# Performance work log

Measured on AMD Instinct MI355X. Metric: run time of the kernel, lower is better.

Reference implementation:

```python
import jax, jax.numpy as jnp
import numpy as np


def setup_inputs() -> dict:
    key = jax.random.key(0)
    ks = jax.random.split(key, 7)
    B, D = 8192, 4096  # D = 64*64 perfect square
    def lin(k, fan_out, fan_in):
        bound = 1.0 / np.sqrt(fan_in)
        kw, kb = jax.random.split(k)
        W = jax.random.uniform(kw, (fan_out, fan_in), jnp.float32, -bound, bound)
        b = jax.random.uniform(kb, (fan_out,), jnp.float32, -bound, bound)
        return W, b
    W1, b1 = lin(ks[1], 512, D)
    W2, b2 = lin(ks[2], 256, 512)
    W3, b3 = lin(ks[3], D, 256)
    x = jax.random.normal(ks[0], (B, D), jnp.float32)
    return {"x": x, "W1": W1, "b1": b1, "W2": W2, "b2": b2, "W3": W3, "b3": b3}


def column_sort(m):
    # torch: sort dim=1; permute(0,2,1) sort dim=1 permute back == sort axis=2; sort dim=1
    m = jnp.sort(m, axis=1)
    m = jnp.sort(m, axis=2)
    m = jnp.sort(m, axis=1)
    return m


def reference(x, W1, b1, W2, b2, W3, b3):
    B, D = x.shape
    n = int(np.sqrt(D))
    xs = column_sort(x.reshape(B, n, n)).reshape(B, D)
    h = jax.nn.relu(xs @ W1.T + b1)
    h = jax.nn.relu(h @ W2.T + b2)
    return h @ W3.T + b3
```

## Files before the change

### kernel.cpp

```cpp
#include <hip/hip_runtime.h>
#include <hip/hip_bf16.h>


#define B_DIM 8192
#define D_DIM 4096
#define H1_DIM 512
#define H2_DIM 256

typedef __attribute__((ext_vector_type(8))) short bf16x8;
typedef __attribute__((ext_vector_type(4))) float f32x4;

__device__ __forceinline__ unsigned short f2bf(float f) {
    union { float f; unsigned u; } v{f};
    unsigned r = v.u + 0x7FFF + ((v.u >> 16) & 1);
    return (unsigned short)(r >> 16);
}

__device__ __forceinline__ void sort64(float v[64]) {
#pragma unroll
    for (int k = 2; k <= 64; k <<= 1) {
#pragma unroll
        for (int j = k >> 1; j > 0; j >>= 1) {
#pragma unroll
            for (int p = 0; p < 32; ++p) {
                const int i  = ((p & ~(j - 1)) << 1) | (p & (j - 1));
                const int ix = i | j;
                const bool up = ((i & k) == 0);
                float a = v[i], b = v[ix];
                float lo = fminf(a, b), hi = fmaxf(a, b);
                v[i]  = up ? lo : hi;
                v[ix] = up ? hi : lo;
            }
        }
    }
}

__global__ __launch_bounds__(64)
void sort_kernel(const float* __restrict__ x, unsigned short* __restrict__ xs)
{
    __shared__ float lds[64 * 68];
    const int b    = blockIdx.x;
    const int lane = threadIdx.x;
    const float* src = x + (size_t)b * D_DIM;
    unsigned short* dst = xs + (size_t)b * D_DIM;

    float4 t[16];
#pragma unroll
    for (int q = 0; q < 16; ++q)
        t[q] = *(const float4*)(src + (q * 64 + lane) * 4);
#pragma unroll
    for (int q = 0; q < 16; ++q) {
        int f = q * 64 + lane;
        *(float4*)&lds[(f >> 4) * 68 + (f & 15) * 4] = t[q];
    }
    __syncthreads();

    float v[64];
#pragma unroll
    for (int i = 0; i < 64; ++i) v[i] = lds[i * 68 + lane];
    sort64(v);

    __syncthreads();
#pragma unroll
    for (int i = 0; i < 64; ++i) lds[i * 68 + lane] = v[i];
    __syncthreads();
#pragma unroll
    for (int q = 0; q < 16; ++q) {
        float4 r = *(const float4*)&lds[lane * 68 + q * 4];
        v[q * 4 + 0] = r.x; v[q * 4 + 1] = r.y;
        v[q * 4 + 2] = r.z; v[q * 4 + 3] = r.w;
    }
    sort64(v);

    __syncthreads();
#pragma unroll
    for (int q = 0; q < 16; ++q) {
        float4 r;
        r.x = v[q * 4 + 0]; r.y = v[q * 4 + 1];
        r.z = v[q * 4 + 2]; r.w = v[q * 4 + 3];
        *(float4*)&lds[lane * 68 + q * 4] = r;
    }
    __syncthreads();
#pragma unroll
    for (int i = 0; i < 64; ++i) v[i] = lds[i * 68 + lane];
    sort64(v);

    __syncthreads();
#pragma unroll
    for (int i = 0; i < 64; ++i) lds[i * 68 + lane] = v[i];
    __syncthreads();
#pragma unroll
    for (int q = 0; q < 16; ++q) {
        int f = q * 64 + lane;
        float4 r = *(const float4*)&lds[(f >> 4) * 68 + (f & 15) * 4];
        ushort4 o;
        o.x = f2bf(r.x); o.y = f2bf(r.y); o.z = f2bf(r.z); o.w = f2bf(r.w);
        *(ushort4*)(dst + f * 4) = o;
    }
}

__global__ __launch_bounds__(256)
void cvt_bf16(const float* __restrict__ src, unsigned short* __restrict__ dst, int n4)
{
    int i = blockIdx.x * blockDim.x + threadIdx.x;
    if (i < n4) {
        float4 v = ((const float4*)src)[i];
        ushort4 o;
        o.x = f2bf(v.x); o.y = f2bf(v.y); o.z = f2bf(v.z); o.w = f2bf(v.w);
        ((ushort4*)dst)[i] = o;
    }
}

template<int BM, int BN, bool RELU, bool OUT_BF16>
__global__ __launch_bounds__(256, 2)
void gemm_mfma(const unsigned short* __restrict__ A,
               const unsigned short* __restrict__ Wt,
               const float* __restrict__ bias,
               void* __restrict__ Cout, int M, int N, int K)
{
    constexpr int BK  = 64;
    constexpr int WTM = BM / 2, WTN = BN / 2;
    constexpr int FM  = WTM / 16, FN = WTN / 16;
    __shared__ unsigned short sA[BM * BK];
    __shared__ unsigned short sB[BN * BK];

    const int tid  = threadIdx.x;
    const int wave = tid >> 6;
    const int lane = tid & 63;
    const int wm   = wave >> 1, wn = wave & 1;
    const int gm0  = blockIdx.y * BM;
    const int gn0  = blockIdx.x * BN;

    const int r_in = lane >> 3;
    const int j_in = lane & 7;

    f32x4 acc[FM][FN] = {};

    for (int k0 = 0; k0 < K; k0 += BK) {
#pragma unroll
        for (int c = 0; c < BM / 32; ++c) {
            int rb  = wave * (BM / 4) + c * 8;
            int r   = rb + r_in;
            int seg = j_in ^ (r & 7);
            const unsigned short* g = A + (size_t)(gm0 + r) * K + k0 + seg * 8;
            __builtin_amdgcn_global_load_lds(
                (const __attribute__((address_space(1))) void*)g,
                (__attribute__((address_space(3))) void*)&sA[rb * 64],
                16, 0, 0);
        }
#pragma unroll
        for (int c = 0; c < BN / 32; ++c) {
            int rb  = wave * (BN / 4) + c * 8;
            int r   = rb + r_in;
            int seg = j_in ^ (r & 7);
            const unsigned short* g = Wt + (size_t)(gn0 + r) * K + k0 + seg * 8;
            __builtin_amdgcn_global_load_lds(
                (const __attribute__((address_space(1))) void*)g,
                (__attribute__((address_space(3))) void*)&sB[rb * 64],
                16, 0, 0);
        }
        __syncthreads();

#pragma unroll
        for (int ks = 0; ks < 2; ++ks) {
            bf16x8 afr[FM], bfr[FN];
#pragma unroll
            for (int i = 0; i < FM; ++i) {
                int m   = wm * WTM + i * 16 + (lane & 15);
                int seg = (ks * 4 + (lane >> 4)) ^ (m & 7);
                afr[i] = *(const bf16x8*)&sA[m * 64 + seg * 8];
            }
#pragma unroll
            for (int j = 0; j < FN; ++j) {
                int n   = wn * WTN + j * 16 + (lane & 15);
                int seg = (ks * 4 + (lane >> 4)) ^ (n & 7);
                bfr[j] = *(const bf16x8*)&sB[n * 64 + seg * 8];
            }
#pragma unroll
            for (int i = 0; i < FM; ++i)
#pragma unroll
                for (int j = 0; j < FN; ++j)
                    acc[i][j] = __builtin_amdgcn_mfma_f32_16x16x32_bf16(
                        afr[i], bfr[j], acc[i][j], 0, 0, 0);
        }
        __syncthreads();
    }

#pragma unroll
    for (int j = 0; j < FN; ++j) {
        int n = gn0 + wn * WTN + j * 16 + (lane & 15);
        float bv = bias[n];
#pragma unroll
        for (int i = 0; i < FM; ++i) {
#pragma unroll
            for (int r = 0; r < 4; ++r) {
                int m = gm0 + wm * WTM + i * 16 + (lane >> 4) * 4 + r;
                float v = acc[i][j][r] + bv;
                if (RELU) v = fmaxf(v, 0.f);
                if (OUT_BF16)
                    ((unsigned short*)Cout)[(size_t)m * N + n] = f2bf(v);
                else
                    ((float*)Cout)[(size_t)m * N + n] = v;
            }
        }
    }
}

extern "C" void kernel_launch(void* const* d_in, const int* in_sizes, int n_in,
                              void* d_out, int out_size, void* d_ws, size_t ws_size,
                              hipStream_t stream)
{
    const float* x  = (const float*)d_in[0];
    const float* W1 = (const float*)d_in[1];
    const float* b1 = (const float*)d_in[2];
    const float* W2 = (const float*)d_in[3];
    const float* b2 = (const float*)d_in[4];
    const float* W3 = (const float*)d_in[5];
    const float* b3 = (const float*)d_in[6];
    float* out = (float*)d_out;

    unsigned short* xs = (unsigned short*)d_out;
    char* ws = (char*)d_ws;
    unsigned short* h1b = (unsigned short*)(ws);
    unsigned short* h2b = (unsigned short*)(ws + (8u  << 20));
    unsigned short* W1b = (unsigned short*)(ws + (12u << 20));
    unsigned short* W2b = (unsigned short*)(ws + (16u << 20));
    unsigned short* W3b = (unsigned short*)(ws + (17u << 20));

    cvt_bf16<<<(H1_DIM * D_DIM / 4 + 255) / 256, 256, 0, stream>>>(W1, W1b, H1_DIM * D_DIM / 4);
    cvt_bf16<<<(H2_DIM * H1_DIM / 4 + 255) / 256, 256, 0, stream>>>(W2, W2b, H2_DIM * H1_DIM / 4);
    cvt_bf16<<<(D_DIM * H2_DIM / 4 + 255) / 256, 256, 0, stream>>>(W3, W3b, D_DIM * H2_DIM / 4);

    sort_kernel<<<B_DIM, 64, 0, stream>>>(x, xs);

    gemm_mfma<128, 64, true, true>
        <<<dim3(H1_DIM / 64, B_DIM / 128), 256, 0, stream>>>(
            xs, W1b, b1, h1b, B_DIM, H1_DIM, D_DIM);

    gemm_mfma<64, 64, true, true>
        <<<dim3(H2_DIM / 64, B_DIM / 64), 256, 0, stream>>>(
            h1b, W2b, b2, h2b, B_DIM, H2_DIM, H1_DIM);

    gemm_mfma<128, 128, false, false>
        <<<dim3(D_DIM / 128, B_DIM / 128), 256, 0, stream>>>(
            h2b, W3b, b3, out, B_DIM, D_DIM, H2_DIM);
}
```

Measured before the change: 391.7 us.

## Sort bf16 order-preserving keys with packed 16-bit min/max network

```diff
diff --git a/kernel.cpp b/kernel.cpp
--- a/kernel.cpp
+++ b/kernel.cpp
@@ -7,6 +7,9 @@
 #define H1_DIM 512
 #define H2_DIM 256
 
+typedef unsigned short u16;
+typedef __attribute__((ext_vector_type(2))) unsigned short u16x2;
+typedef __attribute__((ext_vector_type(2))) short i16x2;
 typedef __attribute__((ext_vector_type(8))) short bf16x8;
 typedef __attribute__((ext_vector_type(4))) float f32x4;
 
@@ -15,86 +18,138 @@
     unsigned r = v.u + 0x7FFF + ((v.u >> 16) & 1);
     return (unsigned short)(r >> 16);
 }
-
-__device__ __forceinline__ void sort64(float v[64]) {
+__device__ __forceinline__ u16 fkey(float f) {
+    u16 bf = f2bf(f);
+    u16 m  = (u16)(((short)bf) >> 15);
+    return (u16)(bf ^ (m | 0x8000));
+}
+__device__ __forceinline__ u16x2 mk2(u16 a, u16 b) { u16x2 r; r.x = a; r.y = b; return r; }
+
+#if defined(__has_builtin) && __has_builtin(__builtin_elementwise_min)
+__device__ __forceinline__ u16x2 pkmin(u16x2 a, u16x2 b) { return __builtin_elementwise_min(a, b); }
+__device__ __forceinline__ u16x2 pkmax(u16x2 a, u16x2 b) { return __builtin_elementwise_max(a, b); }
+#else
+__device__ __forceinline__ u16x2 pkmin(u16x2 a, u16x2 b) {
+    return mk2(a.x < b.x ? a.x : b.x, a.y < b.y ? a.y : b.y);
+}
+__device__ __forceinline__ u16x2 pkmax(u16x2 a, u16x2 b) {
+    return mk2(a.x > b.x ? a.x : b.x, a.y > b.y ? a.y : b.y);
+}
+#endif
+
+__device__ __forceinline__ void sortnet(u16x2 v[32]) {
 #pragma unroll
     for (int k = 2; k <= 64; k <<= 1) {
 #pragma unroll
-        for (int j = k >> 1; j > 0; j >>= 1) {
-#pragma unroll
-            for (int p = 0; p < 32; ++p) {
-                const int i  = ((p & ~(j - 1)) << 1) | (p & (j - 1));
-                const int ix = i | j;
-                const bool up = ((i & k) == 0);
-                float a = v[i], b = v[ix];
-                float lo = fminf(a, b), hi = fmaxf(a, b);
-                v[i]  = up ? lo : hi;
-                v[ix] = up ? hi : lo;
+        for (int j = k >> 1; j >= 1; j >>= 1) {
+            if (j == 32) {
+#pragma unroll
+                for (int p = 0; p < 32; ++p) {
+                    u16x2 sw = mk2(v[p].y, v[p].x);
+                    u16x2 mn = pkmin(v[p], sw), mx = pkmax(v[p], sw);
+                    v[p] = mk2(mn.x, mx.y);
+                }
+            } else {
+#pragma unroll
+                for (int p = 0; p < 32; ++p) {
+                    if (p & j) continue;
+                    const int q = p | j;
+                    const bool upx = ((p & k) == 0);
+                    const bool upy = (((p + 32) & k) == 0);
+                    u16x2 mn = pkmin(v[p], v[q]), mx = pkmax(v[p], v[q]);
+                    if (upx == upy) {
+                        v[p] = upx ? mn : mx;
+                        v[q] = upx ? mx : mn;
+                    } else {
+                        v[p] = mk2(mn.x, mx.y);
+                        v[q] = mk2(mx.x, mn.y);
+                    }
+                }
             }
         }
     }
 }
 
-__global__ __launch_bounds__(64)
-void sort_kernel(const float* __restrict__ x, unsigned short* __restrict__ xs)
+#define SRT 66
+__global__ __launch_bounds__(128)
+void sort_kernel(const float* __restrict__ x, u16* __restrict__ xs)
 {
-    __shared__ float lds[64 * 68];
-    const int b    = blockIdx.x;
-    const int lane = threadIdx.x;
-    const float* src = x + (size_t)b * D_DIM;
-    unsigned short* dst = xs + (size_t)b * D_DIM;
+    __shared__ u16 smem[2 * 64 * SRT];
+    const int wave = threadIdx.x >> 6;
+    const int lane = threadIdx.x & 63;
+    u16* s = smem + wave * 64 * SRT;
+    const int b = blockIdx.x * 2 + wave;
+    const float* src = x  + (size_t)b * D_DIM;
+    u16*         dst = xs + (size_t)b * D_DIM;
 
     float4 t[16];
 #pragma unroll
-    for (int q = 0; q < 16; ++q)
-        t[q] = *(const float4*)(src + (q * 64 + lane) * 4);
-#pragma unroll
-    for (int q = 0; q < 16; ++q) {
-        int f = q * 64 + lane;
-        *(float4*)&lds[(f >> 4) * 68 + (f & 15) * 4] = t[q];
-    }
-    __syncthreads();
-
-    float v[64];
-#pragma unroll
-    for (int i = 0; i < 64; ++i) v[i] = lds[i * 68 + lane];
-    sort64(v);
-
-    __syncthreads();
-#pragma unroll
-    for (int i = 0; i < 64; ++i) lds[i * 68 + lane] = v[i];
-    __syncthreads();
-#pragma unroll
-    for (int q = 0; q < 16; ++q) {
-        float4 r = *(const float4*)&lds[lane * 68 + q * 4];
-        v[q * 4 + 0] = r.x; v[q * 4 + 1] = r.y;
-        v[q * 4 + 2] = r.z; v[q * 4 + 3] = r.w;
-    }
-    sort64(v);
-
-    __syncthreads();
-#pragma unroll
-    for (int q = 0; q < 16; ++q) {
-        float4 r;
-        r.x = v[q * 4 + 0]; r.y = v[q * 4 + 1];
-        r.z = v[q * 4 + 2]; r.w = v[q * 4 + 3];
-        *(float4*)&lds[lane * 68 + q * 4] = r;
-    }
-    __syncthreads();
-#pragma unroll
-    for (int i = 0; i < 64; ++i) v[i] = lds[i * 68 + lane];
-    sort64(v);
-
-    __syncthreads();
-#pragma unroll
-    for (int i = 0; i < 64; ++i) lds[i * 68 + lane] = v[i];
-    __syncthreads();
-#pragma unroll
-    for (int q = 0; q < 16; ++q) {
-        int f = q * 64 + lane;
-        float4 r = *(const float4*)&lds[(f >> 4) * 68 + (f & 15) * 4];
-        ushort4 o;
-        o.x = f2bf(r.x); o.y = f2bf(r.y); o.z = f2bf(r.z); o.w = f2bf(r.w);
+    for (int qq = 0; qq < 16; ++qq)
+        t[qq] = *(const float4*)(src + (qq * 64 + lane) * 4);
+#pragma unroll
+    for (int qq = 0; qq < 16; ++qq) {
+        int f = qq * 64 + lane, r = f >> 4, c0 = (f & 15) * 4;
+        *(u16x2*)&s[r * SRT + c0]     = mk2(fkey(t[qq].x), fkey(t[qq].y));
+        *(u16x2*)&s[r * SRT + c0 + 2] = mk2(fkey(t[qq].z), fkey(t[qq].w));
+    }
+    __syncthreads();
+
+    u16x2 v[32];
+#pragma unroll
+    for (int p = 0; p < 32; ++p)
+        v[p] = mk2(s[p * SRT + lane], s[(p + 32) * SRT + lane]);
+    sortnet(v);
+
+    __syncthreads();
+    {
+        const int pos = (lane & 31) * 2 + (lane >> 5);
+#pragma unroll
+        for (int p = 0; p < 32; ++p) {
+            s[p * SRT + pos]        = v[p].x;
+            s[(p + 32) * SRT + pos] = v[p].y;
+        }
+    }
+    __syncthreads();
+
+#pragma unroll
+    for (int p = 0; p < 32; ++p)
+        v[p] = *(const u16x2*)&s[lane * SRT + p * 2];
+    sortnet(v);
+
+    __syncthreads();
+#pragma unroll
+    for (int p = 0; p < 32; ++p) {
+        s[lane * SRT + p]      = v[p].x;
+        s[lane * SRT + p + 32] = v[p].y;
+    }
+    __syncthreads();
+
+#pragma unroll
+    for (int p = 0; p < 32; ++p)
+        v[p] = mk2(s[p * SRT + lane], s[(p + 32) * SRT + lane]);
+    sortnet(v);
+
+#pragma unroll
+    for (int p = 0; p < 32; ++p) {
+        i16x2 sh = ((i16x2)v[p]) >> 15;
+        u16x2 m  = (u16x2)sh;
+        u16x2 c8; c8.x = 0x8000; c8.y = 0x8000;
+        v[p] = v[p] ^ ((~m) | c8);
+    }
+
+    __syncthreads();
+#pragma unroll
+    for (int p = 0; p < 32; ++p) {
+        s[p * SRT + lane]        = v[p].x;
+        s[(p + 32) * SRT + lane] = v[p].y;
+    }
+    __syncthreads();
+#pragma unroll
+    for (int qq = 0; qq < 16; ++qq) {
+        int f = qq * 64 + lane, r = f >> 4, c0 = (f & 15) * 4;
+        u16x2 a = *(const u16x2*)&s[r * SRT + c0];
+        u16x2 c = *(const u16x2*)&s[r * SRT + c0 + 2];
+        ushort4 o; o.x = a.x; o.y = a.y; o.z = c.x; o.w = c.y;
         *(ushort4*)(dst + f * 4) = o;
     }
 }
@@ -219,7 +274,7 @@
     const float* b3 = (const float*)d_in[6];
     float* out = (float*)d_out;
 
-    unsigned short* xs = (unsigned short*)d_out;
+    u16* xs = (u16*)d_out;
     char* ws = (char*)d_ws;
     unsigned short* h1b = (unsigned short*)(ws);
     unsigned short* h2b = (unsigned short*)(ws + (8u  << 20));
@@ -227,18 +282,18 @@
     unsigned short* W2b = (unsigned short*)(ws + (16u << 20));
     unsigned short* W3b = (unsigned short*)(ws + (17u << 20));
 
+    sort_kernel<<<B_DIM / 2, 128, 0, stream>>>(x, xs);
+
     cvt_bf16<<<(H1_DIM * D_DIM / 4 + 255) / 256, 256, 0, stream>>>(W1, W1b, H1_DIM * D_DIM / 4);
     cvt_bf16<<<(H2_DIM * H1_DIM / 4 + 255) / 256, 256, 0, stream>>>(W2, W2b, H2_DIM * H1_DIM / 4);
     cvt_bf16<<<(D_DIM * H2_DIM / 4 + 255) / 256, 256, 0, stream>>>(W3, W3b, D_DIM * H2_DIM / 4);
 
-    sort_kernel<<<B_DIM, 64, 0, stream>>>(x, xs);
-
     gemm_mfma<128, 64, true, true>
         <<<dim3(H1_DIM / 64, B_DIM / 128), 256, 0, stream>>>(
             xs, W1b, b1, h1b, B_DIM, H1_DIM, D_DIM);
 
-    gemm_mfma<64, 64, true, true>
-        <<<dim3(H2_DIM / 64, B_DIM / 64), 256, 0, stream>>>(
+    gemm_mfma<128, 64, true, true>
+        <<<dim3(H2_DIM / 64, B_DIM / 128), 256, 0, stream>>>(
             h1b, W2b, b2, h2b, B_DIM, H2_DIM, H1_DIM);
 
     gemm_mfma<128, 128, false, false>
```

New measurement: 388.8 us. No clear change (-0.7%).

## Sort two rows per block using packed bf16 keys with pk_min/max

Applied to the files above, without the earlier changes.

```diff
diff --git a/kernel.cpp b/kernel.cpp
--- a/kernel.cpp
+++ b/kernel.cpp
@@ -7,100 +7,139 @@
 #define H1_DIM 512
 #define H2_DIM 256
 
+typedef unsigned int u32;
+typedef unsigned short u16;
+typedef __attribute__((ext_vector_type(2))) short i16x2;
 typedef __attribute__((ext_vector_type(8))) short bf16x8;
 typedef __attribute__((ext_vector_type(4))) float f32x4;
 
-__device__ __forceinline__ unsigned short f2bf(float f) {
+__device__ __forceinline__ u16 f2bf(float f) {
     union { float f; unsigned u; } v{f};
     unsigned r = v.u + 0x7FFF + ((v.u >> 16) & 1);
-    return (unsigned short)(r >> 16);
-}
-
-__device__ __forceinline__ void sort64(float v[64]) {
+    return (u16)(r >> 16);
+}
+
+__device__ __forceinline__ u32 pkmin(u32 a, u32 b) {
+    u32 d; asm("v_pk_min_u16 %0, %1, %2" : "=v"(d) : "v"(a), "v"(b)); return d;
+}
+__device__ __forceinline__ u32 pkmax(u32 a, u32 b) {
+    u32 d; asm("v_pk_max_u16 %0, %1, %2" : "=v"(d) : "v"(a), "v"(b)); return d;
+}
+__device__ __forceinline__ u32 pkashr15(u32 a) {
+    union { u32 u; i16x2 v; } x; x.u = a;
+    x.v = x.v >> 15;
+    return x.u;
+}
+
+__device__ __forceinline__ u32 key2(float fa, float fb) {
+    union { __hip_bfloat162 h; u32 u; } cv;
+    cv.h = __float22bfloat162_rn(float2{fa, fb});
+    u32 bb = cv.u;
+    return bb ^ (pkashr15(bb) | 0x80008000u);
+}
+
+__device__ __forceinline__ void sortnet64(u32 v[64]) {
 #pragma unroll
     for (int k = 2; k <= 64; k <<= 1) {
 #pragma unroll
         for (int j = k >> 1; j > 0; j >>= 1) {
 #pragma unroll
-            for (int p = 0; p < 32; ++p) {
-                const int i  = ((p & ~(j - 1)) << 1) | (p & (j - 1));
-                const int ix = i | j;
+            for (int i = 0; i < 64; ++i) {
+                if (i & j) continue;
+                const int q = i | j;
                 const bool up = ((i & k) == 0);
-                float a = v[i], b = v[ix];
-                float lo = fminf(a, b), hi = fmaxf(a, b);
-                v[i]  = up ? lo : hi;
-                v[ix] = up ? hi : lo;
+                u32 mn = pkmin(v[i], v[q]);
+                u32 mx = pkmax(v[i], v[q]);
+                v[i] = up ? mn : mx;
+                v[q] = up ? mx : mn;
             }
         }
     }
 }
 
 __global__ __launch_bounds__(64)
-void sort_kernel(const float* __restrict__ x, unsigned short* __restrict__ xs)
-{
-    __shared__ float lds[64 * 68];
+void sort_kernel(const float* __restrict__ x, u16* __restrict__ xs)
+{
+    __shared__ u32 S[64 * 64];
+    const int lane = threadIdx.x;
     const int b    = blockIdx.x;
-    const int lane = threadIdx.x;
-    const float* src = x + (size_t)b * D_DIM;
-    unsigned short* dst = xs + (size_t)b * D_DIM;
-
-    float4 t[16];
-#pragma unroll
-    for (int q = 0; q < 16; ++q)
-        t[q] = *(const float4*)(src + (q * 64 + lane) * 4);
+    const float4* A4 = (const float4*)(x + (size_t)(2 * b)     * D_DIM);
+    const float4* B4 = (const float4*)(x + (size_t)(2 * b + 1) * D_DIM);
+    u16* dstA = xs + (size_t)(2 * b)     * D_DIM;
+    u16* dstB = xs + (size_t)(2 * b + 1) * D_DIM;
+
 #pragma unroll
     for (int q = 0; q < 16; ++q) {
         int f = q * 64 + lane;
-        *(float4*)&lds[(f >> 4) * 68 + (f & 15) * 4] = t[q];
-    }
-    __syncthreads();
-
-    float v[64];
-#pragma unroll
-    for (int i = 0; i < 64; ++i) v[i] = lds[i * 68 + lane];
-    sort64(v);
-
-    __syncthreads();
-#pragma unroll
-    for (int i = 0; i < 64; ++i) lds[i * 68 + lane] = v[i];
-    __syncthreads();
-#pragma unroll
-    for (int q = 0; q < 16; ++q) {
-        float4 r = *(const float4*)&lds[lane * 68 + q * 4];
-        v[q * 4 + 0] = r.x; v[q * 4 + 1] = r.y;
-        v[q * 4 + 2] = r.z; v[q * 4 + 3] = r.w;
-    }
-    sort64(v);
-
-    __syncthreads();
-#pragma unroll
-    for (int q = 0; q < 16; ++q) {
-        float4 r;
-        r.x = v[q * 4 + 0]; r.y = v[q * 4 + 1];
-        r.z = v[q * 4 + 2]; r.w = v[q * 4 + 3];
-        *(float4*)&lds[lane * 68 + q * 4] = r;
-    }
-    __syncthreads();
-#pragma unroll
-    for (int i = 0; i < 64; ++i) v[i] = lds[i * 68 + lane];
-    sort64(v);
-
-    __syncthreads();
-#pragma unroll
-    for (int i = 0; i < 64; ++i) lds[i * 68 + lane] = v[i];
-    __syncthreads();
+        float4 a = A4[f], c = B4[f];
+        int r = f >> 4, s = f & 15;
+        uint4 w;
+        w.x = key2(a.x, c.x); w.y = key2(a.y, c.y);
+        w.z = key2(a.z, c.z); w.w = key2(a.w, c.w);
+        *(uint4*)(S + r * 64 + ((s ^ (r & 15)) << 2)) = w;
+    }
+    __syncthreads();
+
+    u32 v[64];
+#pragma unroll
+    for (int p = 0; p < 64; ++p)
+        v[p] = S[p * 64 + (((lane >> 2) ^ (p & 15)) << 2) + (lane & 3)];
+    sortnet64(v);
+    __syncthreads();
+#pragma unroll
+    for (int p = 0; p < 64; ++p)
+        S[p * 64 + (((lane >> 2) ^ (p & 15)) << 2) + (lane & 3)] = v[p];
+    __syncthreads();
+
+#pragma unroll
+    for (int q = 0; q < 16; ++q) {
+        uint4 w = *(const uint4*)(S + lane * 64 + ((q ^ (lane & 15)) << 2));
+        v[4 * q + 0] = w.x; v[4 * q + 1] = w.y;
+        v[4 * q + 2] = w.z; v[4 * q + 3] = w.w;
+    }
+    sortnet64(v);
+    __syncthreads();
+#pragma unroll
+    for (int q = 0; q < 16; ++q) {
+        uint4 w;
+        w.x = v[4 * q + 0]; w.y = v[4 * q + 1];
+        w.z = v[4 * q + 2]; w.w = v[4 * q + 3];
+        *(uint4*)(S + lane * 64 + ((q ^ (lane & 15)) << 2)) = w;
+    }
+    __syncthreads();
+
+#pragma unroll
+    for (int p = 0; p < 64; ++p)
+        v[p] = S[p * 64 + (((lane >> 2) ^ (p & 15)) << 2) + (lane & 3)];
+    sortnet64(v);
+
+#pragma unroll
+    for (int p = 0; p < 64; ++p)
+        v[p] = v[p] ^ (~pkashr15(v[p]) | 0x80008000u);
+
+    __syncthreads();
+#pragma unroll
+    for (int p = 0; p < 64; ++p)
+        S[p * 64 + (((lane >> 2) ^ (p & 15)) << 2) + (lane & 3)] = v[p];
+    __syncthreads();
+
 #pragma unroll
     for (int q = 0; q < 16; ++q) {
         int f = q * 64 + lane;
-        float4 r = *(const float4*)&lds[(f >> 4) * 68 + (f & 15) * 4];
-        ushort4 o;
-        o.x = f2bf(r.x); o.y = f2bf(r.y); o.z = f2bf(r.z); o.w = f2bf(r.w);
-        *(ushort4*)(dst + f * 4) = o;
+        int r = f >> 4, s = f & 15;
+        uint4 w = *(const uint4*)(S + r * 64 + ((s ^ (r & 15)) << 2));
+        uint2 oa, ob;
+        oa.x = (w.x & 0xFFFFu) | (w.y << 16);
+        oa.y = (w.z & 0xFFFFu) | (w.w << 16);
+        ob.x = (w.x >> 16) | (w.y & 0xFFFF0000u);
+        ob.y = (w.z >> 16) | (w.w & 0xFFFF0000u);
+        *(uint2*)(dstA + r * 64 + s * 4) = oa;
+        *(uint2*)(dstB + r * 64 + s * 4) = ob;
     }
 }
 
 __global__ __launch_bounds__(256)
-void cvt_bf16(const float* __restrict__ src, unsigned short* __restrict__ dst, int n4)
+void cvt_bf16(const float* __restrict__ src, u16* __restrict__ dst, int n4)
 {
     int i = blockIdx.x * blockDim.x + threadIdx.x;
     if (i < n4) {
@@ -112,17 +151,16 @@
 }
 
 template<int BM, int BN, bool RELU, bool OUT_BF16>
-__global__ __launch_bounds__(256, 2)
-void gemm_mfma(const unsigned short* __restrict__ A,
-               const unsigned short* __restrict__ Wt,
-               const float* __restrict__ bias,
-               void* __restrict__ Cout, int M, int N, int K)
+__device__ __forceinline__
+void gemm_body(const u16* __restrict__ A, const u16* __restrict__ Wt,
+               const float* __restrict__ bias, void* __restrict__ Cout,
+               int M, int N, int K)
 {
     constexpr int BK  = 64;
     constexpr int WTM = BM / 2, WTN = BN / 2;
     constexpr int FM  = WTM / 16, FN = WTN / 16;
-    __shared__ unsigned short sA[BM * BK];
-    __shared__ unsigned short sB[BN * BK];
+    __shared__ u16 sA[BM * BK];
+    __shared__ u16 sB[BN * BK];
 
     const int tid  = threadIdx.x;
     const int wave = tid >> 6;
@@ -142,7 +180,7 @@
             int rb  = wave * (BM / 4) + c * 8;
             int r   = rb + r_in;
             int seg = j_in ^ (r & 7);
-            const unsigned short* g = A + (size_t)(gm0 + r) * K + k0 + seg * 8;
+            const u16* g = A + (size_t)(gm0 + r) * K + k0 + seg * 8;
             __builtin_amdgcn_global_load_lds(
                 (const __attribute__((address_space(1))) void*)g,
                 (__attribute__((address_space(3))) void*)&sA[rb * 64],
@@ -153,7 +191,7 @@
             int rb  = wave * (BN / 4) + c * 8;
             int r   = rb + r_in;
             int seg = j_in ^ (r & 7);
-            const unsigned short* g = Wt + (size_t)(gn0 + r) * K + k0 + seg * 8;
+            const u16* g = Wt + (size_t)(gn0 + r) * K + k0 + seg * 8;
             __builtin_amdgcn_global_load_lds(
                 (const __attribute__((address_space(1))) void*)g,
                 (__attribute__((address_space(3))) void*)&sB[rb * 64],
@@ -195,16 +233,26 @@
 #pragma unroll
             for (int r = 0; r < 4; ++r) {
                 int m = gm0 + wm * WTM + i * 16 + (lane >> 4) * 4 + r;
-                float v = acc[i][j][r] + bv;
-                if (RELU) v = fmaxf(v, 0.f);
+                float vv = acc[i][j][r] + bv;
+                if (RELU) vv = fmaxf(vv, 0.f);
                 if (OUT_BF16)
-                    ((unsigned short*)Cout)[(size_t)m * N + n] = f2bf(v);
+                    ((u16*)Cout)[(size_t)m * N + n] = f2bf(vv);
                 else
-                    ((float*)Cout)[(size_t)m * N + n] = v;
-            }
-        }
-    }
-}
+                    ((float*)Cout)[(size_t)m * N + n] = vv;
+            }
+        }
+    }
+}
+
+__global__ __launch_bounds__(256, 2)
+void gemm1_xs_w1(const u16* A, const u16* Wt, const float* bias, void* C,
+                 int M, int N, int K) { gemm_body<128, 64, true, true >(A, Wt, bias, C, M, N, K); }
+__global__ __launch_bounds__(256, 2)
+void gemm2_h1_w2(const u16* A, const u16* Wt, const float* bias, void* C,
+                 int M, int N, int K) { gemm_body<128, 64, true, true >(A, Wt, bias, C, M, N, K); }
+__global__ __launch_bounds__(256, 2)
+void gemm3_h2_w3(const u16* A, const u16* Wt, const float* bias, void* C,
+                 int M, int N, int K) { gemm_body<128, 128, false, false>(A, Wt, bias, C, M, N, K); }
 
 extern "C" void kernel_launch(void* const* d_in, const int* in_sizes, int n_in,
                               void* d_out, int out_size, void* d_ws, size_t ws_size,
@@ -217,31 +265,27 @@
     const float* b2 = (const float*)d_in[4];
     const float* W3 = (const float*)d_in[5];
     const float* b3 = (const float*)d_in[6];
-    float* out = (float*)d_out;
-
-    unsigned short* xs = (unsigned short*)d_out;
+
+    u16* xs = (u16*)d_out;
     char* ws = (char*)d_ws;
-    unsigned short* h1b = (unsigned short*)(ws);
-    unsigned short* h2b = (unsigned short*)(ws + (8u  << 20));
-    unsigned short* W1b = (unsigned short*)(ws + (12u << 20));
-    unsigned short* W2b = (unsigned short*)(ws + (16u << 20));
-    unsigned short* W3b = (unsigned short*)(ws + (17u << 20));
+    u16* h1b = (u16*)(ws);
+    u16* h2b = (u16*)(ws + (8u  << 20));
+    u16* W1b = (u16*)(ws + (12u << 20));
+    u16* W2b = (u16*)(ws + (16u << 20));
+    u16* W3b = (u16*)(ws + (17u << 20));
+
+    sort_kernel<<<B_DIM / 2, 64, 0, stream>>>(x, xs);
 
     cvt_bf16<<<(H1_DIM * D_DIM / 4 + 255) / 256, 256, 0, stream>>>(W1, W1b, H1_DIM * D_DIM / 4);
     cvt_bf16<<<(H2_DIM * H1_DIM / 4 + 255) / 256, 256, 0, stream>>>(W2, W2b, H2_DIM * H1_DIM / 4);
     cvt_bf16<<<(D_DIM * H2_DIM / 4 + 255) / 256, 256, 0, stream>>>(W3, W3b, D_DIM * H2_DIM / 4);
 
-    sort_kernel<<<B_DIM, 64, 0, stream>>>(x, xs);
-
-    gemm_mfma<128, 64, true, true>
-        <<<dim3(H1_DIM / 64, B_DIM / 128), 256, 0, stream>>>(
-            xs, W1b, b1, h1b, B_DIM, H1_DIM, D_DIM);
-
-    gemm_mfma<64, 64, true, true>
-        <<<dim3(H2_DIM / 64, B_DIM / 64), 256, 0, stream>>>(
-            h1b, W2b, b2, h2b, B_DIM, H2_DIM, H1_DIM);
-
-    gemm_mfma<128, 128, false, false>
-        <<<dim3(D_DIM / 128, B_DIM / 128), 256, 0, stream>>>(
-            h2b, W3b, b3, out, B_DIM, D_DIM, H2_DIM);
-}
+    gemm1_xs_w1<<<dim3(H1_DIM / 64, B_DIM / 128), 256, 0, stream>>>(
+        xs, W1b, b1, h1b, B_DIM, H1_DIM, D_DIM);
+
+    gemm2_h1_w2<<<dim3(H2_DIM / 64, B_DIM / 128), 256, 0, stream>>>(
+        h1b, W2b, b2, h2b, B_DIM, H2_DIM, H1_DIM);
+
+    gemm3_h2_w3<<<dim3(D_DIM / 128, B_DIM / 128), 256, 0, stream>>>(
+        h2b, W3b, b3, (float*)d_out, B_DIM, D_DIM, H2_DIM);
+}
```

After: 389.7 us. Within noise of the previous version (-0.5%).
